# Kernel tuning notes

Measured on AMD Instinct MI355X. Metric: run time of the kernel, lower is better.

Reference implementation:

```python
import jax, jax.numpy as jnp
import numpy as np

B, N, K, C = 8, 4096, 16, 64
OUT = [128, 128, 128]
BN_EPS = 1e-3


def setup_inputs() -> dict:
    key = jax.random.key(0)
    ks = jax.random.split(key, 8)
    inp = {
        "points1": jax.random.normal(ks[0], (B, 3, N), jnp.float32),
        "points2": jax.random.normal(ks[1], (B, 3, N), jnp.float32),
        "features1": jax.random.normal(ks[2], (B, C, N), jnp.float32),
        "features2": jax.random.normal(ks[3], (B, C, N), jnp.float32),
    }
    dims = [2 * C + 3] + OUT  # [131, 128, 128, 128]
    for i in range(len(OUT)):
        kw = jax.random.fold_in(ks[4], i)
        inp[f"W{i}"] = jax.random.normal(kw, (dims[i + 1], dims[i]), jnp.float32) / np.sqrt(dims[i]).astype(np.float32)
        inp[f"b{i}"] = jnp.zeros((dims[i + 1],), jnp.float32)
        inp[f"gamma{i}"] = jnp.ones((dims[i + 1],), jnp.float32)
        inp[f"beta{i}"] = jnp.zeros((dims[i + 1],), jnp.float32)
    return inp


def _knn_group(points2, points1, features2):
    # points*: [B, 3, N].  For each query in points1, find K nearest in points2.
    d = jnp.sum((points1[:, :, :, None] - points2[:, :, None, :]) ** 2, axis=1)  # [B, Nq, Ns]
    _, idx = jax.lax.top_k(-d, K)  # [B, Nq, K]
    idx_b = idx[:, None, :, :]  # [B, 1, Nq, K] broadcasts over channel dim
    xyz_g = jnp.take_along_axis(points2[:, :, None, :], idx_b, axis=3)      # [B, 3, Nq, K]
    rel_xyz = xyz_g - points1[:, :, :, None]                                # relative coords
    feat_g = jnp.take_along_axis(features2[:, :, None, :], idx_b, axis=3)  # [B, C, Nq, K]
    return jnp.concatenate([rel_xyz, feat_g], axis=1)  # [B, C+3, Nq, K]


def _conv_bn_relu(x, W, b, gamma, beta):
    # 1x1 conv == per-position channel matmul; BN in training mode (batch stats, biased var)
    x = jnp.einsum('oc,bcnk->bonk', W, x) + b[None, :, None, None]
    mu = jnp.mean(x, axis=(0, 2, 3), keepdims=True)
    var = jnp.var(x, axis=(0, 2, 3), keepdims=True)
    x = (x - mu) * jax.lax.rsqrt(var + BN_EPS)
    x = x * gamma[None, :, None, None] + beta[None, :, None, None]
    return jax.nn.relu(x)


def reference(points1, points2, features1, features2,
              W0, b0, gamma0, beta0,
              W1, b1, gamma1, beta1,
              W2, b2, gamma2, beta2):
    g = _knn_group(points2, points1, features2)                       # [B, C+3, N, K]
    f1 = jnp.broadcast_to(features1[:, :, :, None], (B, C, N, K))     # expand over neighbors
    x = jnp.concatenate([g, f1], axis=1)                              # [B, 2C+3, N, K]
    x = _conv_bn_relu(x, W0, b0, gamma0, beta0)
    x = _conv_bn_relu(x, W1, b1, gamma1, beta1)
    x = _conv_bn_relu(x, W2, b2, gamma2, beta2)
    return jnp.max(x, axis=3)                                         # [B, OUT[-1], N]
```

## Files before the change

kernel.cpp:

```cpp
#include <hip/hip_runtime.h>

#define B_ 8
#define N_ 4096
#define K_ 16
#define C_ 64
#define NK_ (N_*K_)
#define M_ (B_*N_*K_)
#define BN_EPS_ 0.001f
#define CH_ 16
#define CS_ (N_/CH_)
#define Q_ (B_*N_)
#define NB1_ (M_/128)

typedef short bf16x8 __attribute__((ext_vector_type(8)));
typedef float f32x4 __attribute__((ext_vector_type(4)));

static __device__ __forceinline__ unsigned short f2bf(float x) {
  unsigned u = __float_as_uint(x);
  unsigned r = (u + 0x7FFFu + ((u >> 16) & 1u)) >> 16;
  return (unsigned short)r;
}
static __device__ __forceinline__ unsigned pk2bf(float a, float b) {
  return (unsigned)f2bf(a) | ((unsigned)f2bf(b) << 16);
}

__global__ __launch_bounds__(256) void pack_pts(const float* __restrict__ p,
                                                float4* __restrict__ pf4) {
  int i = blockIdx.x * 256 + threadIdx.x;
  int b = i >> 12;
  int n = i & (N_ - 1);
  const float* base = p + (size_t)b * 3 * N_;
  pf4[i] = make_float4(base[n], base[N_ + n], base[2 * N_ + n], 0.f);
}

__global__ __launch_bounds__(256) void wcvt(const float* __restrict__ W,
                                            unsigned short* __restrict__ Wb) {
  int i = blockIdx.x * 256 + threadIdx.x;
  Wb[i] = f2bf(W[i]);
}

__global__ void make_w0at(const float* __restrict__ W0, float* __restrict__ w0at) {
  int o = threadIdx.x;
  for (int d = 0; d < 3; ++d) w0at[d * 128 + o] = W0[o * 131 + d];
}

__global__ __launch_bounds__(64) void knn_part(const float4* __restrict__ p1f4,
                                               const float4* __restrict__ p2f4,
                                               float* __restrict__ pvals) {
  int lane = threadIdx.x;
  int blk = blockIdx.x;
  int chunk = blk & (CH_ - 1);
  int grp = (blk >> 4) & 63;
  int b = blk >> 10;
  int n1 = (grp << 6) + lane;
  int q = (b << 12) + n1;
  float4 qv = p1f4[q];
  float ax = qv.x, ay = qv.y, az = qv.z;
  const float4* pb = p2f4 + ((size_t)b << 12) + chunk * CS_;

  float s[16];
  #pragma unroll
  for (int i = 0; i < 16; ++i) s[i] = 3.0e38f;

  #pragma unroll 8
  for (int t = 0; t < CS_; ++t) {
    float4 c = pb[t];
    float dx = ax - c.x, dy = ay - c.y, dz = az - c.z;
    float d = __fadd_rn(__fadd_rn(__fmul_rn(dx, dx), __fmul_rn(dy, dy)), __fmul_rn(dz, dz));
    #pragma unroll
    for (int i = 0; i < 15; ++i) s[i] = __builtin_amdgcn_fmed3f(s[i], s[i + 1], d);
    s[15] = fminf(s[15], d);
  }
  #pragma unroll
  for (int i = 0; i < 16; ++i) pvals[(size_t)(chunk * 16 + i) * Q_ + q] = s[i];
}

__global__ __launch_bounds__(256) void knn_merge(const float* __restrict__ pvals,
                                                 float* __restrict__ Tarr) {
  int q = blockIdx.x * 256 + threadIdx.x;
  float s[16];
  #pragma unroll
  for (int i = 0; i < 16; ++i) s[i] = 3.0e38f;
  #pragma unroll 8
  for (int t = 0; t < CH_ * 16; ++t) {
    float d = pvals[(size_t)t * Q_ + q];
    #pragma unroll
    for (int i = 0; i < 15; ++i) s[i] = __builtin_amdgcn_fmed3f(s[i], s[i + 1], d);
    s[15] = fminf(s[15], d);
  }
  Tarr[q] = s[0];
}

__global__ __launch_bounds__(64) void knn_cand(const float4* __restrict__ p1f4,
                                               const float4* __restrict__ p2f4,
                                               const float* __restrict__ Tarr,
                                               int* __restrict__ cidx,
                                               int* __restrict__ ccnt) {
  int lane = threadIdx.x;
  int blk = blockIdx.x;
  int chunk = blk & (CH_ - 1);
  int grp = (blk >> 4) & 63;
  int b = blk >> 10;
  int n1 = (grp << 6) + lane;
  int q = (b << 12) + n1;
  float4 qq = p1f4[q];
  float ax = qq.x, ay = qq.y, az = qq.z;
  const float4* pb = p2f4 + ((size_t)b << 12) + chunk * CS_;
  float T = Tarr[q];
  int cnt = 0;
  int base = (q * CH_ + chunk) * 16;
  #pragma unroll 4
  for (int t = 0; t < CS_; ++t) {
    float4 c = pb[t];
    float dx = ax - c.x, dy = ay - c.y, dz = az - c.z;
    float d = __fadd_rn(__fadd_rn(__fmul_rn(dx, dx), __fmul_rn(dy, dy)), __fmul_rn(dz, dz));
    if (d <= T && cnt < 16) { cidx[base + cnt] = chunk * CS_ + t; ++cnt; }
  }
  ccnt[q * CH_ + chunk] = cnt;
}

__global__ __launch_bounds__(256) void knn_combine(const int* __restrict__ cidx,
                                                   const int* __restrict__ ccnt,
                                                   int* __restrict__ idxout) {
  int q = blockIdx.x * 256 + threadIdx.x;
  int tot = 0;
  int ob = q * 16;
  for (int c = 0; c < CH_; ++c) {
    int m = ccnt[q * CH_ + c];
    const int* src = cidx + (size_t)(q * CH_ + c) * 16;
    for (int i = 0; i < m && tot < 16; ++i) idxout[ob + tot++] = src[i];
  }
}

__global__ __launch_bounds__(256) void pkern(const float* __restrict__ f,
                                             const float* __restrict__ W0,
                                             const float* __restrict__ bias,
                                             const float4* __restrict__ pf4,
                                             const float* __restrict__ w0at,
                                             float sgn,
                                             float* __restrict__ P, int coff) {
  __shared__ float fx[32 * 65];
  __shared__ __align__(16) float Wl[64 * 132];
  int tid = threadIdx.x;
  int bn0 = blockIdx.x * 32;
  int b = bn0 >> 12, nb0 = bn0 & (N_ - 1);

  for (int u = tid; u < 32 * 64; u += 256) {
    int c = u >> 5, nl = u & 31;
    fx[nl * 65 + c] = f[((size_t)b * C_ + c) * N_ + nb0 + nl];
  }
  for (int u = tid; u < 128 * 64; u += 256) {
    int o = u >> 6, c = u & 63;
    Wl[c * 132 + o] = W0[o * 131 + coff + c];
  }
  __syncthreads();

  int og = tid & 15, np_ = tid >> 4;
  int o0 = og * 8;
  int na = np_ * 2, nb = na + 1;
  float acc0[8], acc1[8];
  #pragma unroll
  for (int j = 0; j < 8; ++j) {
    float bv = bias ? bias[o0 + j] : 0.f;
    acc0[j] = bv; acc1[j] = bv;
  }
  for (int c = 0; c < 64; ++c) {
    float x0 = fx[na * 65 + c], x1 = fx[nb * 65 + c];
    float4 wa = *(const float4*)&Wl[c * 132 + o0];
    float4 wb = *(const float4*)&Wl[c * 132 + o0 + 4];
    float w[8] = {wa.x, wa.y, wa.z, wa.w, wb.x, wb.y, wb.z, wb.w};
    #pragma unroll
    for (int j = 0; j < 8; ++j) {
      acc0[j] = fmaf(x0, w[j], acc0[j]);
      acc1[j] = fmaf(x1, w[j], acc1[j]);
    }
  }
  float4 pa = pf4[bn0 + na], pb_ = pf4[bn0 + nb];
  #pragma unroll
  for (int j = 0; j < 8; ++j) {
    float wx = w0at[o0 + j], wy = w0at[128 + o0 + j], wz = w0at[256 + o0 + j];
    acc0[j] += sgn * (wx * pa.x + wy * pa.y + wz * pa.z);
    acc1[j] += sgn * (wx * pb_.x + wy * pb_.y + wz * pb_.z);
  }
  float* Pa = P + (size_t)(bn0 + na) * 128 + o0;
  float* Pb = P + (size_t)(bn0 + nb) * 128 + o0;
  *(float4*)Pa = make_float4(acc0[0], acc0[1], acc0[2], acc0[3]);
  *(float4*)(Pa + 4) = make_float4(acc0[4], acc0[5], acc0[6], acc0[7]);
  *(float4*)Pb = make_float4(acc1[0], acc1[1], acc1[2], acc1[3]);
  *(float4*)(Pb + 4) = make_float4(acc1[4], acc1[5], acc1[6], acc1[7]);
}

__global__ __launch_bounds__(256) void stats0_kernel(
    const float* __restrict__ A, const float* __restrict__ Bv,
    const int* __restrict__ idx, float* __restrict__ part) {
  __shared__ float sred[4 * 128 * 2];
  int tid = threadIdx.x;
  int R0 = blockIdx.x * 128;
  int b = R0 >> 16;
  int n0 = (R0 & (NK_ - 1)) >> 4;
  int cc = (tid & 15) * 8;
  int r0l = tid >> 4;

  int jj[8];
  #pragma unroll
  for (int p = 0; p < 8; ++p) jj[p] = idx[R0 + r0l + p * 16];

  float ssum[8], ssq[8];
  #pragma unroll
  for (int u = 0; u < 8; ++u) { ssum[u] = 0.f; ssq[u] = 0.f; }

  #pragma unroll
  for (int p = 0; p < 8; ++p) {
    const float* Ar = A + (size_t)((b << 12) + n0 + p) * 128 + cc;
    const float* Br = Bv + (size_t)((b << 12) + jj[p]) * 128 + cc;
    float4 a0 = *(const float4*)Ar, a1 = *(const float4*)(Ar + 4);
    float4 b0v = *(const float4*)Br, b1v = *(const float4*)(Br + 4);
    float av[8], bv[8];
    *(float4*)&av[0] = a0; *(float4*)&av[4] = a1;
    *(float4*)&bv[0] = b0v; *(float4*)&bv[4] = b1v;
    #pragma unroll
    for (int u = 0; u < 8; ++u) {
      float x = av[u] + bv[u];
      ssum[u] += x;
      ssq[u] = fmaf(x, x, ssq[u]);
    }
  }
  int w = tid >> 6, lane = tid & 63;
  #pragma unroll
  for (int u = 0; u < 8; ++u) {
    ssum[u] += __shfl_xor(ssum[u], 16);
    ssum[u] += __shfl_xor(ssum[u], 32);
    ssq[u] += __shfl_xor(ssq[u], 16);
    ssq[u] += __shfl_xor(ssq[u], 32);
  }
  if (lane < 16) {
    #pragma unroll
    for (int u = 0; u < 8; ++u) {
      sred[(w * 128 + lane * 8 + u) * 2] = ssum[u];
      sred[(w * 128 + lane * 8 + u) * 2 + 1] = ssq[u];
    }
  }
  __syncthreads();
  if (tid < 128) {
    float a = 0.f, q2 = 0.f;
    #pragma unroll
    for (int ww = 0; ww < 4; ++ww) {
      a += sred[(ww * 128 + tid) * 2];
      q2 += sred[(ww * 128 + tid) * 2 + 1];
    }
    part[(size_t)tid * NB1_ + blockIdx.x] = a;
    part[(size_t)(128 + tid) * NB1_ + blockIdx.x] = q2;
  }
}

__global__ __launch_bounds__(256) void reduce_stats(const float* __restrict__ part,
                                                    int nb, float* __restrict__ statso) {
  int s = blockIdx.x;
  int tid = threadIdx.x;
  const float* src = part + (size_t)s * nb;
  float a = 0.f;
  for (int i = tid; i < nb; i += 256) a += src[i];
  a += __shfl_xor(a, 1);  a += __shfl_xor(a, 2);  a += __shfl_xor(a, 4);
  a += __shfl_xor(a, 8);  a += __shfl_xor(a, 16); a += __shfl_xor(a, 32);
  __shared__ float red[4];
  if ((tid & 63) == 0) red[tid >> 6] = a;
  __syncthreads();
  if (tid == 0) statso[s] = red[0] + red[1] + red[2] + red[3];
}

__global__ void bnfin_kernel(const float* __restrict__ stats, const float* __restrict__ gamma,
                             const float* __restrict__ beta, float* __restrict__ bnp) {
  int o = threadIdx.x;
  const float invM = 1.0f / (float)M_;
  float mean = stats[o] * invM;
  float var = stats[128 + o] * invM - mean * mean;
  float s = gamma[o] * rsqrtf(var + BN_EPS_);
  bnp[o] = s;
  bnp[128 + o] = beta[o] - mean * s;
}

__global__ __launch_bounds__(256) void bnprep(const float* __restrict__ Bv,
                                              const float* __restrict__ bnp0,
                                              unsigned short* __restrict__ Bv16) {
  int i = blockIdx.x * 256 + threadIdx.x;
  size_t e0 = (size_t)i * 8;
  int c0 = (int)(e0 & 127);
  float4 s0 = *(const float4*)(bnp0 + c0), s1 = *(const float4*)(bnp0 + c0 + 4);
  float4 v0 = *(const float4*)(Bv + e0), v1 = *(const float4*)(Bv + e0 + 4);
  uint4 pk;
  pk.x = pk2bf(s0.x * v0.x, s0.y * v0.y);
  pk.y = pk2bf(s0.z * v0.z, s0.w * v0.w);
  pk.z = pk2bf(s1.x * v1.x, s1.y * v1.y);
  pk.w = pk2bf(s1.z * v1.z, s1.w * v1.w);
  *(uint4*)(Bv16 + e0) = pk;
}

static __device__ __forceinline__ void stage_x(
    unsigned short* Xs, const float* A, const unsigned short* Bv16,
    const int* idx, const float* bnp0, int R0, int b, int n0, int tid) {
  int cc = (tid & 15) * 8;
  int r0l = tid >> 4;
  float svv[8], tvv[8];
  *(float4*)&svv[0] = *(const float4*)(bnp0 + cc);       *(float4*)&svv[4] = *(const float4*)(bnp0 + cc + 4);
  *(float4*)&tvv[0] = *(const float4*)(bnp0 + 128 + cc); *(float4*)&tvv[4] = *(const float4*)(bnp0 + 132 + cc);
  int jj[8];
  #pragma unroll
  for (int p = 0; p < 8; ++p) jj[p] = idx[R0 + r0l + p * 16];
  #pragma unroll
  for (int g = 0; g < 2; ++g) {
    uint4 bvp[4];
    float4 aa[4], ab[4];
    #pragma unroll
    for (int t = 0; t < 4; ++t) {
      int p = g * 4 + t;
      bvp[t] = *(const uint4*)(Bv16 + (size_t)((b << 12) + jj[p]) * 128 + cc);
      const float* Ar = A + (size_t)((b << 12) + n0 + p) * 128 + cc;
      aa[t] = *(const float4*)Ar;
      ab[t] = *(const float4*)(Ar + 4);
    }
    #pragma unroll
    for (int t = 0; t < 4; ++t) {
      int p = g * 4 + t;
      float av[8];
      *(float4*)&av[0] = aa[t]; *(float4*)&av[4] = ab[t];
      unsigned bw[4] = {bvp[t].x, bvp[t].y, bvp[t].z, bvp[t].w};
      float y[8];
      #pragma unroll
      for (int u = 0; u < 8; ++u) {
        unsigned wv = bw[u >> 1];
        float bvf = __uint_as_float((u & 1) ? (wv & 0xFFFF0000u) : (wv << 16));
        y[u] = fmaxf(fmaf(svv[u], av[u], tvv[u]) + bvf, 0.f);
      }
      uint4 pk;
      pk.x = pk2bf(y[0], y[1]); pk.y = pk2bf(y[2], y[3]);
      pk.z = pk2bf(y[4], y[5]); pk.w = pk2bf(y[6], y[7]);
      *(uint4*)&Xs[(r0l + p * 16) * 136 + cc] = pk;
    }
  }
}

__global__ __launch_bounds__(256) void layer1_stats(
    const float* __restrict__ A, const unsigned short* __restrict__ Bv16,
    const int* __restrict__ idx, const float* __restrict__ bnp0,
    const unsigned short* __restrict__ W1b, const float* __restrict__ b1,
    float* __restrict__ part) {
  __shared__ __align__(16) unsigned short Xs[128 * 136];
  __shared__ float sred[4 * 128 * 2];
  int tid = threadIdx.x;
  int R0 = blockIdx.x * 128;
  int b = R0 >> 16;
  int n0 = (R0 & (NK_ - 1)) >> 4;

  stage_x(Xs, A, Bv16, idx, bnp0, R0, b, n0, tid);
  __syncthreads();

  int w = tid >> 6, lane = tid & 63;
  int m16 = lane & 15, qd = lane >> 4;
  f32x4 acc[2][8];
  #pragma unroll
  for (int mt = 0; mt < 2; ++mt)
    #pragma unroll
    for (int nt = 0; nt < 8; ++nt) acc[mt][nt] = (f32x4){0.f, 0.f, 0.f, 0.f};

  const unsigned short* Ab = &Xs[(w * 32 + m16) * 136 + qd * 8];
  const unsigned short* Bb = W1b + m16 * 128 + qd * 8;
  #pragma unroll 1
  for (int q = 0; q < 4; ++q) {
    bf16x8 A0 = *(const bf16x8*)(Ab + q * 32);
    bf16x8 A1 = *(const bf16x8*)(Ab + 16 * 136 + q * 32);
    #pragma unroll
    for (int nt = 0; nt < 8; ++nt) {
      bf16x8 Bv_ = *(const bf16x8*)(Bb + nt * 16 * 128 + q * 32);
      acc[0][nt] = __builtin_amdgcn_mfma_f32_16x16x32_bf16(A0, Bv_, acc[0][nt], 0, 0, 0);
      acc[1][nt] = __builtin_amdgcn_mfma_f32_16x16x32_bf16(A1, Bv_, acc[1][nt], 0, 0, 0);
    }
  }

  float ssum[8], ssq[8];
  #pragma unroll
  for (int nt = 0; nt < 8; ++nt) { ssum[nt] = 0.f; ssq[nt] = 0.f; }
  #pragma unroll
  for (int nt = 0; nt < 8; ++nt) {
    float bb = b1[nt * 16 + m16];
    #pragma unroll
    for (int mt = 0; mt < 2; ++mt) {
      #pragma unroll
      for (int rg = 0; rg < 4; ++rg) {
        float y = acc[mt][nt][rg] + bb;
        ssum[nt] += y;
        ssq[nt] = fmaf(y, y, ssq[nt]);
      }
    }
  }
  #pragma unroll
  for (int nt = 0; nt < 8; ++nt) {
    ssum[nt] += __shfl_xor(ssum[nt], 16);
    ssum[nt] += __shfl_xor(ssum[nt], 32);
    ssq[nt] += __shfl_xor(ssq[nt], 16);
    ssq[nt] += __shfl_xor(ssq[nt], 32);
  }
  if (lane < 16) {
    #pragma unroll
    for (int nt = 0; nt < 8; ++nt) {
      sred[(w * 128 + nt * 16 + lane) * 2] = ssum[nt];
      sred[(w * 128 + nt * 16 + lane) * 2 + 1] = ssq[nt];
    }
  }
  __syncthreads();
  if (tid < 128) {
    float a = 0.f, q2 = 0.f;
    #pragma unroll
    for (int ww = 0; ww < 4; ++ww) {
      a += sred[(ww * 128 + tid) * 2];
      q2 += sred[(ww * 128 + tid) * 2 + 1];
    }
    part[(size_t)tid * NB1_ + blockIdx.x] = a;
    part[(size_t)(128 + tid) * NB1_ + blockIdx.x] = q2;
  }
}

__global__ __launch_bounds__(256) void layer2_fused(
    const float* __restrict__ A, const unsigned short* __restrict__ Bv16,
    const int* __restrict__ idx, const float* __restrict__ bnp0,
    const unsigned short* __restrict__ W1b, const float* __restrict__ b1,
    const float* __restrict__ bnp1, const unsigned short* __restrict__ W2b,
    const float* __restrict__ b2, float* __restrict__ ymaxo,
    float* __restrict__ ymino, float* __restrict__ part) {
  __shared__ __align__(16) unsigned short Xs[128 * 136];
  __shared__ float sred[4 * 128 * 2];
  int tid = threadIdx.x;
  int R0 = blockIdx.x * 128;
  int b = R0 >> 16;
  int n0 = (R0 & (NK_ - 1)) >> 4;

  stage_x(Xs, A, Bv16, idx, bnp0, R0, b, n0, tid);
  __syncthreads();

  int w = tid >> 6, lane = tid & 63;
  int m16 = lane & 15, qd = lane >> 4;
  f32x4 acc[2][8];
  #pragma unroll
  for (int mt = 0; mt < 2; ++mt)
    #pragma unroll
    for (int nt = 0; nt < 8; ++nt) acc[mt][nt] = (f32x4){0.f, 0.f, 0.f, 0.f};

  const unsigned short* Ab = &Xs[(w * 32 + m16) * 136 + qd * 8];
  const unsigned short* Bb = W1b + m16 * 128 + qd * 8;
  #pragma unroll 1
  for (int q = 0; q < 4; ++q) {
    bf16x8 A0 = *(const bf16x8*)(Ab + q * 32);
    bf16x8 A1 = *(const bf16x8*)(Ab + 16 * 136 + q * 32);
    #pragma unroll
    for (int nt = 0; nt < 8; ++nt) {
      bf16x8 Bv_ = *(const bf16x8*)(Bb + nt * 16 * 128 + q * 32);
      acc[0][nt] = __builtin_amdgcn_mfma_f32_16x16x32_bf16(A0, Bv_, acc[0][nt], 0, 0, 0);
      acc[1][nt] = __builtin_amdgcn_mfma_f32_16x16x32_bf16(A1, Bv_, acc[1][nt], 0, 0, 0);
    }
  }
  __syncthreads();

  #pragma unroll
  for (int nt = 0; nt < 8; ++nt) {
    int col = nt * 16 + m16;
    float sc = bnp1[col];
    float tc = fmaf(sc, b1[col], bnp1[128 + col]);
    #pragma unroll
    for (int mt = 0; mt < 2; ++mt) {
      #pragma unroll
      for (int rg = 0; rg < 4; ++rg) {
        float y = fmaxf(fmaf(sc, acc[mt][nt][rg], tc), 0.f);
        Xs[(w * 32 + mt * 16 + qd * 4 + rg) * 136 + col] = f2bf(y);
      }
    }
  }
  __syncthreads();

  #pragma unroll
  for (int mt = 0; mt < 2; ++mt)
    #pragma unroll
    for (int nt = 0; nt < 8; ++nt) acc[mt][nt] = (f32x4){0.f, 0.f, 0.f, 0.f};

  const unsigned short* Bb2 = W2b + m16 * 128 + qd * 8;
  #pragma unroll 1
  for (int q = 0; q < 4; ++q) {
    bf16x8 A0 = *(const bf16x8*)(Ab + q * 32);
    bf16x8 A1 = *(const bf16x8*)(Ab + 16 * 136 + q * 32);
    #pragma unroll
    for (int nt = 0; nt < 8; ++nt) {
      bf16x8 Bv_ = *(const bf16x8*)(Bb2 + nt * 16 * 128 + q * 32);
      acc[0][nt] = __builtin_amdgcn_mfma_f32_16x16x32_bf16(A0, Bv_, acc[0][nt], 0, 0, 0);
      acc[1][nt] = __builtin_amdgcn_mfma_f32_16x16x32_bf16(A1, Bv_, acc[1][nt], 0, 0, 0);
    }
  }

  float ssum[8], ssq[8], mxv[2][8], mnv[2][8];
  #pragma unroll
  for (int nt = 0; nt < 8; ++nt) { ssum[nt] = 0.f; ssq[nt] = 0.f; }
  #pragma unroll
  for (int nt = 0; nt < 8; ++nt) {
    float bb = b2[nt * 16 + m16];
    #pragma unroll
    for (int mt = 0; mt < 2; ++mt) {
      float y0 = acc[mt][nt][0] + bb;
      float mx = y0, mn = y0, su = y0, sq = y0 * y0;
      #pragma unroll
      for (int rg = 1; rg < 4; ++rg) {
        float y = acc[mt][nt][rg] + bb;
        mx = fmaxf(mx, y); mn = fminf(mn, y);
        su += y; sq = fmaf(y, y, sq);
      }
      mxv[mt][nt] = mx; mnv[mt][nt] = mn;
      ssum[nt] += su; ssq[nt] += sq;
    }
  }
  #pragma unroll
  for (int nt = 0; nt < 8; ++nt)
    #pragma unroll
    for (int mt = 0; mt < 2; ++mt) {
      mxv[mt][nt] = fmaxf(mxv[mt][nt], __shfl_xor(mxv[mt][nt], 16));
      mxv[mt][nt] = fmaxf(mxv[mt][nt], __shfl_xor(mxv[mt][nt], 32));
      mnv[mt][nt] = fminf(mnv[mt][nt], __shfl_xor(mnv[mt][nt], 16));
      mnv[mt][nt] = fminf(mnv[mt][nt], __shfl_xor(mnv[mt][nt], 32));
    }
  if (lane < 16) {
    #pragma unroll
    for (int mt = 0; mt < 2; ++mt) {
      int n = n0 + w * 2 + mt;
      size_t base = ((size_t)(b << 12) + n) * 128;
      #pragma unroll
      for (int nt = 0; nt < 8; ++nt) {
        ymaxo[base + nt * 16 + lane] = mxv[mt][nt];
        ymino[base + nt * 16 + lane] = mnv[mt][nt];
      }
    }
  }
  #pragma unroll
  for (int nt = 0; nt < 8; ++nt) {
    ssum[nt] += __shfl_xor(ssum[nt], 16);
    ssum[nt] += __shfl_xor(ssum[nt], 32);
    ssq[nt] += __shfl_xor(ssq[nt], 16);
    ssq[nt] += __shfl_xor(ssq[nt], 32);
  }
  if (lane < 16) {
    #pragma unroll
    for (int nt = 0; nt < 8; ++nt) {
      sred[(w * 128 + nt * 16 + lane) * 2] = ssum[nt];
      sred[(w * 128 + nt * 16 + lane) * 2 + 1] = ssq[nt];
    }
  }
  __syncthreads();
  if (tid < 128) {
    float a = 0.f, q2 = 0.f;
    #pragma unroll
    for (int ww = 0; ww < 4; ++ww) {
      a += sred[(ww * 128 + tid) * 2];
      q2 += sred[(ww * 128 + tid) * 2 + 1];
    }
    part[(size_t)tid * NB1_ + blockIdx.x] = a;
    part[(size_t)(128 + tid) * NB1_ + blockIdx.x] = q2;
  }
}

__global__ __launch_bounds__(256) void final_kernel(const float* __restrict__ ymaxo,
                                                    const float* __restrict__ ymino,
                                                    const float* __restrict__ bnp2,
                                                    float* __restrict__ out) {
  __shared__ float T[64 * 129];
  int tid = threadIdx.x;
  int b = blockIdx.x >> 6;
  int n0 = (blockIdx.x & 63) * 64;
  for (int u = tid; u < 64 * 128; u += 256) {
    int nl = u >> 7, o = u & 127;
    size_t base = ((size_t)(b << 12) + n0 + nl) * 128 + o;
    float s = bnp2[o], t = bnp2[128 + o];
    float v = fmaf(s, (s >= 0.f ? ymaxo[base] : ymino[base]), t);
    T[nl * 129 + o] = fmaxf(v, 0.f);
  }
  __syncthreads();
  for (int u = tid; u < 64 * 128; u += 256) {
    int o = u >> 6, nl = u & 63;
    out[((size_t)b * 128 + o) * N_ + n0 + nl] = T[nl * 129 + o];
  }
}

extern "C" void kernel_launch(void* const* d_in, const int* in_sizes, int n_in,
                              void* d_out, int out_size, void* d_ws, size_t ws_size,
                              hipStream_t stream) {
  (void)in_sizes; (void)n_in; (void)out_size; (void)ws_size;
  const float* points1 = (const float*)d_in[0];
  const float* points2 = (const float*)d_in[1];
  const float* features1 = (const float*)d_in[2];
  const float* features2 = (const float*)d_in[3];
  const float* W0 = (const float*)d_in[4];
  const float* b0 = (const float*)d_in[5];
  const float* g0 = (const float*)d_in[6];
  const float* be0 = (const float*)d_in[7];
  const float* W1 = (const float*)d_in[8];
  const float* b1 = (const float*)d_in[9];
  const float* g1 = (const float*)d_in[10];
  const float* be1 = (const float*)d_in[11];
  const float* W2 = (const float*)d_in[12];
  const float* b2 = (const float*)d_in[13];
  const float* g2 = (const float*)d_in[14];
  const float* be2 = (const float*)d_in[15];
  float* out = (float*)d_out;

  char* ws = (char*)d_ws;
  size_t off = 0;
  auto alloc = [&](size_t bytes) -> void* {
    void* p = ws + off;
    off += (bytes + 255) & ~(size_t)255;
    return p;
  };
  int* idx = (int*)alloc((size_t)M_ * 4);
  float4* p1f4 = (float4*)alloc((size_t)B_ * N_ * 16);
  float4* p2f4 = (float4*)alloc((size_t)B_ * N_ * 16);
  float* A = (float*)alloc((size_t)B_ * N_ * 128 * 4);
  float* Bv = (float*)alloc((size_t)B_ * N_ * 128 * 4);
  unsigned short* Bv16 = (unsigned short*)alloc((size_t)B_ * N_ * 128 * 2);
  unsigned short* W1b = (unsigned short*)alloc(128 * 128 * 2);
  unsigned short* W2b = (unsigned short*)alloc(128 * 128 * 2);
  float* w0at = (float*)alloc(3 * 128 * 4);
  float* stats = (float*)alloc(3 * 256 * 4);
  float* bnp = (float*)alloc(3 * 256 * 4);
  float* ymaxo = (float*)alloc((size_t)B_ * N_ * 128 * 4);
  float* ymino = (float*)alloc((size_t)B_ * N_ * 128 * 4);
  float* pvals = (float*)alloc((size_t)CH_ * 16 * Q_ * 4);
  int* cidx = (int*)alloc((size_t)Q_ * CH_ * 16 * 4);
  int* ccnt = (int*)alloc((size_t)Q_ * CH_ * 4);
  float* Tarr = (float*)alloc((size_t)Q_ * 4);

  float* part0 = ymaxo;
  float* part1 = ymino;
  float* part2 = pvals;

  pack_pts<<<B_ * N_ / 256, 256, 0, stream>>>(points1, p1f4);
  pack_pts<<<B_ * N_ / 256, 256, 0, stream>>>(points2, p2f4);
  wcvt<<<64, 256, 0, stream>>>(W1, W1b);
  wcvt<<<64, 256, 0, stream>>>(W2, W2b);
  make_w0at<<<1, 128, 0, stream>>>(W0, w0at);

  knn_part<<<B_ * 64 * CH_, 64, 0, stream>>>(p1f4, p2f4, pvals);
  knn_merge<<<Q_ / 256, 256, 0, stream>>>(pvals, Tarr);
  knn_cand<<<B_ * 64 * CH_, 64, 0, stream>>>(p1f4, p2f4, Tarr, cidx, ccnt);
  knn_combine<<<Q_ / 256, 256, 0, stream>>>(cidx, ccnt, idx);

  pkern<<<B_ * N_ / 32, 256, 0, stream>>>(features1, W0, b0, p1f4, w0at, -1.f, A, 67);
  pkern<<<B_ * N_ / 32, 256, 0, stream>>>(features2, W0, nullptr, p2f4, w0at, 1.f, Bv, 3);

  stats0_kernel<<<NB1_, 256, 0, stream>>>(A, Bv, idx, part0);
  reduce_stats<<<256, 256, 0, stream>>>(part0, NB1_, stats);
  bnfin_kernel<<<1, 128, 0, stream>>>(stats, g0, be0, bnp);

  bnprep<<<M_ / 256, 256, 0, stream>>>(Bv, bnp, Bv16);

  layer1_stats<<<NB1_, 256, 0, stream>>>(A, Bv16, idx, bnp, W1b, b1, part1);
  reduce_stats<<<256, 256, 0, stream>>>(part1, NB1_, stats + 256);
  bnfin_kernel<<<1, 128, 0, stream>>>(stats + 256, g1, be1, bnp + 256);

  layer2_fused<<<NB1_, 256, 0, stream>>>(A, Bv16, idx, bnp, W1b, b1, bnp + 256,
                                         W2b, b2, ymaxo, ymino, part2);
  reduce_stats<<<256, 256, 0, stream>>>(part2, NB1_, stats + 512);
  bnfin_kernel<<<1, 128, 0, stream>>>(stats + 512, g2, be2, bnp + 512);

  final_kernel<<<B_ * N_ / 64, 256, 0, stream>>>(ymaxo, ymino, bnp + 512, out);
}
```

Baseline: 609.1 us.

## Materialize grouped layer-0 pre-activations in bf16 and stream them linearly

The stats pass now writes the gathered layer-0 pre-activation (A + Bv[idx]) as bf16 into a 128 MB buffer that reuses the kNN scratch space, and computes batch statistics on the rounded values. The two MLP passes read this buffer contiguously instead of gathering fp32 A and bf16 Bv rows through idx each time, so the bnprep kernel goes away. LDS staging switches from padded rows to an XOR-swizzled layout, and the reduction scratch is aliased onto the same LDS to cut shared memory use. The trade is an extra 128 MB write plus bf16 rounding before the BN affine, which changes numerics slightly.

New measurement: 623.0 us. +2.3%, slower.

```diff
diff --git a/kernel.cpp b/kernel.cpp
--- a/kernel.cpp
+++ b/kernel.cpp
@@ -190,9 +190,10 @@
   *(float4*)(Pb + 4) = make_float4(acc1[4], acc1[5], acc1[6], acc1[7]);
 }
 
-__global__ __launch_bounds__(256) void stats0_kernel(
+__global__ __launch_bounds__(256) void gstats_kernel(
     const float* __restrict__ A, const float* __restrict__ Bv,
-    const int* __restrict__ idx, float* __restrict__ part) {
+    const int* __restrict__ idx, unsigned short* __restrict__ x0b,
+    float* __restrict__ part) {
   __shared__ float sred[4 * 128 * 2];
   int tid = threadIdx.x;
   int R0 = blockIdx.x * 128;
@@ -213,17 +214,24 @@
   for (int p = 0; p < 8; ++p) {
     const float* Ar = A + (size_t)((b << 12) + n0 + p) * 128 + cc;
     const float* Br = Bv + (size_t)((b << 12) + jj[p]) * 128 + cc;
-    float4 a0 = *(const float4*)Ar, a1 = *(const float4*)(Ar + 4);
-    float4 b0v = *(const float4*)Br, b1v = *(const float4*)(Br + 4);
     float av[8], bv[8];
-    *(float4*)&av[0] = a0; *(float4*)&av[4] = a1;
-    *(float4*)&bv[0] = b0v; *(float4*)&bv[4] = b1v;
+    *(float4*)&av[0] = *(const float4*)Ar;  *(float4*)&av[4] = *(const float4*)(Ar + 4);
+    *(float4*)&bv[0] = *(const float4*)Br;  *(float4*)&bv[4] = *(const float4*)(Br + 4);
+    unsigned short h[8];
     #pragma unroll
     for (int u = 0; u < 8; ++u) {
       float x = av[u] + bv[u];
-      ssum[u] += x;
-      ssq[u] = fmaf(x, x, ssq[u]);
-    }
+      h[u] = f2bf(x);
+      float q = __uint_as_float((unsigned)h[u] << 16);
+      ssum[u] += q;
+      ssq[u] = fmaf(q, q, ssq[u]);
+    }
+    uint4 pk;
+    pk.x = (unsigned)h[0] | ((unsigned)h[1] << 16);
+    pk.y = (unsigned)h[2] | ((unsigned)h[3] << 16);
+    pk.z = (unsigned)h[4] | ((unsigned)h[5] << 16);
+    pk.w = (unsigned)h[6] | ((unsigned)h[7] << 16);
+    *(uint4*)(x0b + (size_t)(R0 + r0l + p * 16) * 128 + cc) = pk;
   }
   int w = tid >> 6, lane = tid & 63;
   #pragma unroll
@@ -279,95 +287,63 @@
   bnp[128 + o] = beta[o] - mean * s;
 }
 
-__global__ __launch_bounds__(256) void bnprep(const float* __restrict__ Bv,
-                                              const float* __restrict__ bnp0,
-                                              unsigned short* __restrict__ Bv16) {
-  int i = blockIdx.x * 256 + threadIdx.x;
-  size_t e0 = (size_t)i * 8;
-  int c0 = (int)(e0 & 127);
-  float4 s0 = *(const float4*)(bnp0 + c0), s1 = *(const float4*)(bnp0 + c0 + 4);
-  float4 v0 = *(const float4*)(Bv + e0), v1 = *(const float4*)(Bv + e0 + 4);
-  uint4 pk;
-  pk.x = pk2bf(s0.x * v0.x, s0.y * v0.y);
-  pk.y = pk2bf(s0.z * v0.z, s0.w * v0.w);
-  pk.z = pk2bf(s1.x * v1.x, s1.y * v1.y);
-  pk.w = pk2bf(s1.z * v1.z, s1.w * v1.w);
-  *(uint4*)(Bv16 + e0) = pk;
-}
-
-static __device__ __forceinline__ void stage_x(
-    unsigned short* Xs, const float* A, const unsigned short* Bv16,
-    const int* idx, const float* bnp0, int R0, int b, int n0, int tid) {
+static __device__ __forceinline__ char* xsa(unsigned short* Xs, int row, int bytecol) {
+  return (char*)Xs + row * 256 + (bytecol ^ ((row & 7) << 4));
+}
+
+static __device__ __forceinline__ void stage_lin(
+    unsigned short* Xs, const unsigned short* x0b, const float* bnp0,
+    int R0, int tid) {
   int cc = (tid & 15) * 8;
   int r0l = tid >> 4;
   float svv[8], tvv[8];
   *(float4*)&svv[0] = *(const float4*)(bnp0 + cc);       *(float4*)&svv[4] = *(const float4*)(bnp0 + cc + 4);
   *(float4*)&tvv[0] = *(const float4*)(bnp0 + 128 + cc); *(float4*)&tvv[4] = *(const float4*)(bnp0 + 132 + cc);
-  int jj[8];
-  #pragma unroll
-  for (int p = 0; p < 8; ++p) jj[p] = idx[R0 + r0l + p * 16];
-  #pragma unroll
-  for (int g = 0; g < 2; ++g) {
-    uint4 bvp[4];
-    float4 aa[4], ab[4];
-    #pragma unroll
-    for (int t = 0; t < 4; ++t) {
-      int p = g * 4 + t;
-      bvp[t] = *(const uint4*)(Bv16 + (size_t)((b << 12) + jj[p]) * 128 + cc);
-      const float* Ar = A + (size_t)((b << 12) + n0 + p) * 128 + cc;
-      aa[t] = *(const float4*)Ar;
-      ab[t] = *(const float4*)(Ar + 4);
-    }
-    #pragma unroll
-    for (int t = 0; t < 4; ++t) {
-      int p = g * 4 + t;
-      float av[8];
-      *(float4*)&av[0] = aa[t]; *(float4*)&av[4] = ab[t];
-      unsigned bw[4] = {bvp[t].x, bvp[t].y, bvp[t].z, bvp[t].w};
-      float y[8];
-      #pragma unroll
-      for (int u = 0; u < 8; ++u) {
-        unsigned wv = bw[u >> 1];
-        float bvf = __uint_as_float((u & 1) ? (wv & 0xFFFF0000u) : (wv << 16));
-        y[u] = fmaxf(fmaf(svv[u], av[u], tvv[u]) + bvf, 0.f);
-      }
-      uint4 pk;
-      pk.x = pk2bf(y[0], y[1]); pk.y = pk2bf(y[2], y[3]);
-      pk.z = pk2bf(y[4], y[5]); pk.w = pk2bf(y[6], y[7]);
-      *(uint4*)&Xs[(r0l + p * 16) * 136 + cc] = pk;
-    }
-  }
-}
-
-__global__ __launch_bounds__(256) void layer1_stats(
-    const float* __restrict__ A, const unsigned short* __restrict__ Bv16,
-    const int* __restrict__ idx, const float* __restrict__ bnp0,
+  #pragma unroll
+  for (int p = 0; p < 8; ++p) {
+    uint4 pv = *(const uint4*)(x0b + (size_t)(R0 + r0l + p * 16) * 128 + cc);
+    float xv[8];
+    xv[0] = __uint_as_float(pv.x << 16); xv[1] = __uint_as_float(pv.x & 0xFFFF0000u);
+    xv[2] = __uint_as_float(pv.y << 16); xv[3] = __uint_as_float(pv.y & 0xFFFF0000u);
+    xv[4] = __uint_as_float(pv.z << 16); xv[5] = __uint_as_float(pv.z & 0xFFFF0000u);
+    xv[6] = __uint_as_float(pv.w << 16); xv[7] = __uint_as_float(pv.w & 0xFFFF0000u);
+    float y[8];
+    #pragma unroll
+    for (int u = 0; u < 8; ++u) y[u] = fmaxf(fmaf(svv[u], xv[u], tvv[u]), 0.f);
+    uint4 pk;
+    pk.x = pk2bf(y[0], y[1]); pk.y = pk2bf(y[2], y[3]);
+    pk.z = pk2bf(y[4], y[5]); pk.w = pk2bf(y[6], y[7]);
+    *(uint4*)xsa(Xs, r0l + p * 16, 16 * (tid & 15)) = pk;
+  }
+}
+
+__global__ __launch_bounds__(256) void pass1_kernel(
+    const unsigned short* __restrict__ x0b, const float* __restrict__ bnp0,
     const unsigned short* __restrict__ W1b, const float* __restrict__ b1,
     float* __restrict__ part) {
-  __shared__ __align__(16) unsigned short Xs[128 * 136];
-  __shared__ float sred[4 * 128 * 2];
+  __shared__ __align__(16) unsigned short Xs[128 * 128];
+  float* sred = (float*)Xs;
   int tid = threadIdx.x;
   int R0 = blockIdx.x * 128;
-  int b = R0 >> 16;
-  int n0 = (R0 & (NK_ - 1)) >> 4;
-
-  stage_x(Xs, A, Bv16, idx, bnp0, R0, b, n0, tid);
+
+  stage_lin(Xs, x0b, bnp0, R0, tid);
   __syncthreads();
 
   int w = tid >> 6, lane = tid & 63;
   int m16 = lane & 15, qd = lane >> 4;
+  int ar = w * 32 + m16;
   f32x4 acc[2][8];
   #pragma unroll
   for (int mt = 0; mt < 2; ++mt)
     #pragma unroll
     for (int nt = 0; nt < 8; ++nt) acc[mt][nt] = (f32x4){0.f, 0.f, 0.f, 0.f};
 
-  const unsigned short* Ab = &Xs[(w * 32 + m16) * 136 + qd * 8];
   const unsigned short* Bb = W1b + m16 * 128 + qd * 8;
   #pragma unroll 1
   for (int q = 0; q < 4; ++q) {
-    bf16x8 A0 = *(const bf16x8*)(Ab + q * 32);
-    bf16x8 A1 = *(const bf16x8*)(Ab + 16 * 136 + q * 32);
+    int bc = 16 * qd + 64 * q;
+    bf16x8 A0 = *(const bf16x8*)xsa(Xs, ar, bc);
+    bf16x8 A1 = *(const bf16x8*)xsa(Xs, ar + 16, bc);
     #pragma unroll
     for (int nt = 0; nt < 8; ++nt) {
       bf16x8 Bv_ = *(const bf16x8*)(Bb + nt * 16 * 128 + q * 32);
@@ -399,6 +375,7 @@
     ssq[nt] += __shfl_xor(ssq[nt], 16);
     ssq[nt] += __shfl_xor(ssq[nt], 32);
   }
+  __syncthreads();
   if (lane < 16) {
     #pragma unroll
     for (int nt = 0; nt < 8; ++nt) {
@@ -419,37 +396,37 @@
   }
 }
 
-__global__ __launch_bounds__(256) void layer2_fused(
-    const float* __restrict__ A, const unsigned short* __restrict__ Bv16,
-    const int* __restrict__ idx, const float* __restrict__ bnp0,
+__global__ __launch_bounds__(256) void pass2_kernel(
+    const unsigned short* __restrict__ x0b, const float* __restrict__ bnp0,
     const unsigned short* __restrict__ W1b, const float* __restrict__ b1,
     const float* __restrict__ bnp1, const unsigned short* __restrict__ W2b,
     const float* __restrict__ b2, float* __restrict__ ymaxo,
     float* __restrict__ ymino, float* __restrict__ part) {
-  __shared__ __align__(16) unsigned short Xs[128 * 136];
-  __shared__ float sred[4 * 128 * 2];
+  __shared__ __align__(16) unsigned short Xs[128 * 128];
+  float* sred = (float*)Xs;
   int tid = threadIdx.x;
   int R0 = blockIdx.x * 128;
   int b = R0 >> 16;
   int n0 = (R0 & (NK_ - 1)) >> 4;
 
-  stage_x(Xs, A, Bv16, idx, bnp0, R0, b, n0, tid);
+  stage_lin(Xs, x0b, bnp0, R0, tid);
   __syncthreads();
 
   int w = tid >> 6, lane = tid & 63;
   int m16 = lane & 15, qd = lane >> 4;
+  int ar = w * 32 + m16;
   f32x4 acc[2][8];
   #pragma unroll
   for (int mt = 0; mt < 2; ++mt)
     #pragma unroll
     for (int nt = 0; nt < 8; ++nt) acc[mt][nt] = (f32x4){0.f, 0.f, 0.f, 0.f};
 
-  const unsigned short* Ab = &Xs[(w * 32 + m16) * 136 + qd * 8];
   const unsigned short* Bb = W1b + m16 * 128 + qd * 8;
   #pragma unroll 1
   for (int q = 0; q < 4; ++q) {
-    bf16x8 A0 = *(const bf16x8*)(Ab + q * 32);
-    bf16x8 A1 = *(const bf16x8*)(Ab + 16 * 136 + q * 32);
+    int bc = 16 * qd + 64 * q;
+    bf16x8 A0 = *(const bf16x8*)xsa(Xs, ar, bc);
+    bf16x8 A1 = *(const bf16x8*)xsa(Xs, ar + 16, bc);
     #pragma unroll
     for (int nt = 0; nt < 8; ++nt) {
       bf16x8 Bv_ = *(const bf16x8*)(Bb + nt * 16 * 128 + q * 32);
@@ -457,7 +434,6 @@
       acc[1][nt] = __builtin_amdgcn_mfma_f32_16x16x32_bf16(A1, Bv_, acc[1][nt], 0, 0, 0);
     }
   }
-  __syncthreads();
 
   #pragma unroll
   for (int nt = 0; nt < 8; ++nt) {
@@ -468,12 +444,12 @@
     for (int mt = 0; mt < 2; ++mt) {
       #pragma unroll
       for (int rg = 0; rg < 4; ++rg) {
+        int row = w * 32 + mt * 16 + qd * 4 + rg;
         float y = fmaxf(fmaf(sc, acc[mt][nt][rg], tc), 0.f);
-        Xs[(w * 32 + mt * 16 + qd * 4 + rg) * 136 + col] = f2bf(y);
+        *(unsigned short*)xsa(Xs, row, 2 * col) = f2bf(y);
       }
     }
   }
-  __syncthreads();
 
   #pragma unroll
   for (int mt = 0; mt < 2; ++mt)
@@ -483,8 +459,9 @@
   const unsigned short* Bb2 = W2b + m16 * 128 + qd * 8;
   #pragma unroll 1
   for (int q = 0; q < 4; ++q) {
-    bf16x8 A0 = *(const bf16x8*)(Ab + q * 32);
-    bf16x8 A1 = *(const bf16x8*)(Ab + 16 * 136 + q * 32);
+    int bc = 16 * qd + 64 * q;
+    bf16x8 A0 = *(const bf16x8*)xsa(Xs, ar, bc);
+    bf16x8 A1 = *(const bf16x8*)xsa(Xs, ar + 16, bc);
     #pragma unroll
     for (int nt = 0; nt < 8; ++nt) {
       bf16x8 Bv_ = *(const bf16x8*)(Bb2 + nt * 16 * 128 + q * 32);
@@ -541,6 +518,7 @@
     ssq[nt] += __shfl_xor(ssq[nt], 16);
     ssq[nt] += __shfl_xor(ssq[nt], 32);
   }
+  __syncthreads();
   if (lane < 16) {
     #pragma unroll
     for (int nt = 0; nt < 8; ++nt) {
@@ -617,7 +595,6 @@
   float4* p2f4 = (float4*)alloc((size_t)B_ * N_ * 16);
   float* A = (float*)alloc((size_t)B_ * N_ * 128 * 4);
   float* Bv = (float*)alloc((size_t)B_ * N_ * 128 * 4);
-  unsigned short* Bv16 = (unsigned short*)alloc((size_t)B_ * N_ * 128 * 2);
   unsigned short* W1b = (unsigned short*)alloc(128 * 128 * 2);
   unsigned short* W2b = (unsigned short*)alloc(128 * 128 * 2);
   float* w0at = (float*)alloc(3 * 128 * 4);
@@ -625,14 +602,16 @@
   float* bnp = (float*)alloc(3 * 256 * 4);
   float* ymaxo = (float*)alloc((size_t)B_ * N_ * 128 * 4);
   float* ymino = (float*)alloc((size_t)B_ * N_ * 128 * 4);
-  float* pvals = (float*)alloc((size_t)CH_ * 16 * Q_ * 4);
-  int* cidx = (int*)alloc((size_t)Q_ * CH_ * 16 * 4);
-  int* ccnt = (int*)alloc((size_t)Q_ * CH_ * 4);
-  float* Tarr = (float*)alloc((size_t)Q_ * 4);
+  char* bigbuf = (char*)alloc((size_t)128 * 1024 * 1024);
+  float* pvals = (float*)bigbuf;
+  int* cidx = (int*)(bigbuf + (size_t)32 * 1024 * 1024);
+  int* ccnt = (int*)(bigbuf + (size_t)64 * 1024 * 1024);
+  float* Tarr = (float*)(bigbuf + (size_t)66 * 1024 * 1024);
+  unsigned short* x0b = (unsigned short*)bigbuf;
 
   float* part0 = ymaxo;
   float* part1 = ymino;
-  float* part2 = pvals;
+  float* part2 = A;
 
   pack_pts<<<B_ * N_ / 256, 256, 0, stream>>>(points1, p1f4);
   pack_pts<<<B_ * N_ / 256, 256, 0, stream>>>(points2, p2f4);
@@ -648,17 +627,15 @@
   pkern<<<B_ * N_ / 32, 256, 0, stream>>>(features1, W0, b0, p1f4, w0at, -1.f, A, 67);
   pkern<<<B_ * N_ / 32, 256, 0, stream>>>(features2, W0, nullptr, p2f4, w0at, 1.f, Bv, 3);
 
-  stats0_kernel<<<NB1_, 256, 0, stream>>>(A, Bv, idx, part0);
+  gstats_kernel<<<NB1_, 256, 0, stream>>>(A, Bv, idx, x0b, part0);
   reduce_stats<<<256, 256, 0, stream>>>(part0, NB1_, stats);
   bnfin_kernel<<<1, 128, 0, stream>>>(stats, g0, be0, bnp);
 
-  bnprep<<<M_ / 256, 256, 0, stream>>>(Bv, bnp, Bv16);
-
-  layer1_stats<<<NB1_, 256, 0, stream>>>(A, Bv16, idx, bnp, W1b, b1, part1);
+  pass1_kernel<<<NB1_, 256, 0, stream>>>(x0b, bnp, W1b, b1, part1);
   reduce_stats<<<256, 256, 0, stream>>>(part1, NB1_, stats + 256);
   bnfin_kernel<<<1, 128, 0, stream>>>(stats + 256, g1, be1, bnp + 256);
 
-  layer2_fused<<<NB1_, 256, 0, stream>>>(A, Bv16, idx, bnp, W1b, b1, bnp + 256,
+  pass2_kernel<<<NB1_, 256, 0, stream>>>(x0b, bnp, W1b, b1, bnp + 256,
                                          W2b, b2, ymaxo, ymino, part2);
   reduce_stats<<<256, 256, 0, stream>>>(part2, NB1_, stats + 512);
   bnfin_kernel<<<1, 128, 0, stream>>>(stats + 512, g2, be2, bnp + 512);
```
